# Kernel optimization log

Measured on AMD Instinct MI355X. Metric: run time of the kernel, lower is better.

The kernel has to match this reference:

```python
import jax, jax.numpy as jnp
import numpy as np

R = 8192        # rays
S_C = 64        # coarse samples per ray
S_F = 128       # fine samples per ray
NEAR, FAR = 2.0, 6.0
HIDDEN = 64
WHITE_BKGD = True
EPS_T = 1e-10   # transmittance eps (matches volumetric_rendering)
EPS_W = 1e-5    # weight-sum padding eps (matches piecewise_constant_pdf)


def setup_inputs() -> dict:
    key = jax.random.key(0)
    k0, k1, k2, k3, k4, k5 = jax.random.split(key, 6)
    return {
        "ray_origins": jax.random.normal(k0, (R, 3), jnp.float32),
        "ray_directions": jax.random.normal(k1, (R, 3), jnp.float32),
        "W1": jax.random.normal(k2, (6, HIDDEN), jnp.float32) * 0.5,
        "b1": jax.random.normal(k3, (HIDDEN,), jnp.float32) * 0.1,
        "W2": jax.random.normal(k4, (HIDDEN, 4), jnp.float32) * 0.3,
        "b2": jax.random.normal(k5, (4,), jnp.float32) * 0.1,
    }


def _mlp(coords, viewdirs, W1, b1, W2, b2):
    # coords: [R,S,3], viewdirs: [R,3] -> raw_rgb [R,S,3], raw_sigma [R,S]
    vd = jnp.broadcast_to(viewdirs[:, None, :], coords.shape)
    x = jnp.concatenate([coords, vd], axis=-1)            # [R,S,6]
    h = jax.nn.relu(jnp.einsum('rsi,ih->rsh', x, W1) + b1)
    out = jnp.einsum('rsh,ho->rso', h, W2) + b2           # [R,S,4]
    return out[..., :3], out[..., 3]


def _volrender(rgb, sigma, z_vals, directions):
    # rgb [R,S,3], sigma [R,S], z_vals [R,S], directions [R,3]
    dists = (z_vals[:, 1:] - z_vals[:, :-1]) * jnp.linalg.norm(directions, axis=-1, keepdims=True)
    alpha = 1.0 - jnp.exp(-sigma[:, :-1] * dists)         # [R,S-1]
    trans = jnp.concatenate([jnp.ones_like(alpha[:, :1]),
                             jnp.cumprod(1.0 - alpha + EPS_T, axis=-1)], axis=-1)
    alpha = jnp.concatenate([alpha, jnp.ones_like(alpha[:, :1])], axis=-1)
    weights = alpha * trans                               # [R,S]
    comp_rgb = jnp.einsum('rs,rsc->rc', weights, rgb)
    acc = weights.sum(-1)
    depth = (weights * z_vals).sum(-1)
    if WHITE_BKGD:
        comp_rgb = comp_rgb + (1.0 - acc)[:, None]
    return comp_rgb, weights, depth


def _piecewise_constant_pdf(bins, weights, num_samples):
    # bins [R,B+1], weights [R,B]; deterministic branch (randomized=False)
    nbins = weights.shape[-1]
    wsum = weights.sum(-1, keepdims=True)
    padding = jnp.maximum(0.0, EPS_W - wsum)
    weights = weights + padding / nbins
    wsum = wsum + padding
    pdf = weights / wsum
    cdf = jnp.minimum(1.0, jnp.cumsum(pdf[:, :-1], axis=-1))
    cdf = jnp.concatenate([jnp.zeros_like(cdf[:, :1]), cdf, jnp.ones_like(cdf[:, :1])], axis=-1)  # [R,B+1]
    u = jnp.linspace(0.0, 1.0 - jnp.finfo(jnp.float32).eps, num_samples)  # [F]
    mask = u[None, None, :] >= cdf[:, :, None]            # [R,B+1,F]

    def find_interval(x):  # x [R,B+1]
        x0 = jnp.max(jnp.where(mask, x[:, :, None], x[:, :1, None]), axis=1)
        x1 = jnp.min(jnp.where(~mask, x[:, :, None], x[:, -1:, None]), axis=1)
        return x0, x1

    bins_g0, bins_g1 = find_interval(bins)
    cdf_g0, cdf_g1 = find_interval(cdf)
    t = jnp.clip(jnp.nan_to_num((u[None, :] - cdf_g0) / (cdf_g1 - cdf_g0), nan=0.0), 0.0, 1.0)
    return jax.lax.stop_gradient(bins_g0 + t * (bins_g1 - bins_g0))  # [R,F]


def reference(ray_origins, ray_directions, W1, b1, W2, b2):
    Rn = ray_origins.shape[0]
    viewdirs = ray_directions / jnp.linalg.norm(ray_directions, axis=-1, keepdims=True)
    # coarse stratification (lindisp=False, randomized=False)
    t = jnp.linspace(0.0, 1.0, S_C)
    z_vals = jnp.broadcast_to(NEAR * (1.0 - t) + FAR * t, (Rn, S_C))
    coords = ray_origins[:, None, :] + z_vals[..., None] * ray_directions[:, None, :]
    raw_rgb, raw_sigma = _mlp(coords, viewdirs, W1, b1, W2, b2)
    rgb, sigma = jax.nn.sigmoid(raw_rgb), jax.nn.relu(raw_sigma)
    coarse_rgb, weights, coarse_depth = _volrender(rgb, sigma, z_vals, ray_directions)
    # hierarchical fine sampling via inverse-CDF over midpoint bins
    z_mid = 0.5 * (z_vals[:, 1:] + z_vals[:, :-1])
    z_samples = _piecewise_constant_pdf(z_mid, weights[:, 1:-1], S_F)
    z_fine = jnp.sort(jnp.concatenate([z_vals, z_samples], axis=-1), axis=-1)  # [R,S_C+S_F]
    coords = ray_origins[:, None, :] + z_fine[..., None] * ray_directions[:, None, :]
    # source falls through to coarse_model in the non-stateful branch; we mirror that (same MLP)
    raw_rgb, raw_sigma = _mlp(coords, viewdirs, W1, b1, W2, b2)
    rgb, sigma = jax.nn.sigmoid(raw_rgb), jax.nn.relu(raw_sigma)
    fine_rgb, _, fine_depth = _volrender(rgb, sigma, z_fine, ray_directions)
    return jnp.concatenate([coarse_rgb, coarse_depth[:, None], fine_rgb, fine_depth[:, None]], axis=-1)  # [R,8]
```

## Files before the change

### kernel.cpp

```cpp
#include <hip/hip_runtime.h>
#include <math.h>


#define RAYS   8192
#define NEARP  2.0f
#define FARP   6.0f
#define EPS_T  1e-10f
#define EPS_W  1e-5f
#define F32EPS 1.1920929e-7f

typedef float v2f __attribute__((ext_vector_type(2)));
__device__ __forceinline__ v2f mk2(float a, float b) { v2f r; r.x = a; r.y = b; return r; }
__device__ __forceinline__ v2f pfma(v2f a, v2f b, v2f c) { return __builtin_elementwise_fma(a, b, c); }
__device__ __forceinline__ v2f pmax0(v2f a) { return __builtin_elementwise_max(a, mk2(0.f, 0.f)); }

__device__ __forceinline__ float zc(int i) {
    const float t = (float)i * (1.0f / 63.0f);
    return NEARP * (1.0f - t) + FARP * t;
}
__device__ __forceinline__ float sigm(float x) { return 1.f / (1.f + __expf(-x)); }

__global__ __launch_bounds__(256) void nerf_kernel(
    const float* __restrict__ ro, const float* __restrict__ rd,
    const float* __restrict__ W1, const float* __restrict__ b1,
    const float* __restrict__ W2, const float* __restrict__ b2,
    float* __restrict__ out)
{
    __shared__ __align__(16) float sA[4][64];
    __shared__ __align__(16) float sB[4][64];
    __shared__ float sCdf[4][64];
    __shared__ float sZc [4][64];
    __shared__ float sZs [4][128];
    __shared__ float sZf [4][192];

    const int tid  = threadIdx.x;
    const int w    = tid >> 6;
    const int lane = tid & 63;
    const int ray  = blockIdx.x * 4 + w;

    const float ox = ro[ray * 3 + 0], oy = ro[ray * 3 + 1], oz = ro[ray * 3 + 2];
    const float dx = rd[ray * 3 + 0], dy = rd[ray * 3 + 1], dz = rd[ray * 3 + 2];
    const float norm = sqrtf(dx * dx + dy * dy + dz * dz);
    const float inv  = 1.f / norm;
    const float vx = dx * inv, vy = dy * inv, vz = dz * inv;

    {
        const float w10 = W1[lane],       w11 = W1[64 + lane],  w12 = W1[128 + lane];
        const float w13 = W1[192 + lane], w14 = W1[256 + lane], w15 = W1[320 + lane];
        float A = b1[lane];
        A = fmaf(vz, w15, A); A = fmaf(vy, w14, A); A = fmaf(vx, w13, A);
        A = fmaf(oz, w12, A); A = fmaf(oy, w11, A); A = fmaf(ox, w10, A);
        const float B = fmaf(dx, w10, fmaf(dy, w11, dz * w12));
        sA[w][lane] = A; sB[w][lane] = B;
    }
    __syncthreads();

    const float4* W2v = (const float4*)W2;
    const float bb0 = b2[0], bb1 = b2[1], bb2 = b2[2], bb3 = b2[3];

    const float z = zc(lane);
    sZc[w][lane] = z;
    const v2f zz = mk2(z, z);
    v2f o01 = mk2(bb0, bb1), o23 = mk2(bb2, bb3);
#pragma unroll 4
    for (int i = 0; i < 16; ++i) {
        const float4 a4 = ((const float4*)sA[w])[i];
        const float4 b4 = ((const float4*)sB[w])[i];
        const float4 q0 = W2v[4 * i + 0], q1 = W2v[4 * i + 1];
        const float4 q2 = W2v[4 * i + 2], q3 = W2v[4 * i + 3];
        const v2f hL = pmax0(pfma(zz, mk2(b4.x, b4.y), mk2(a4.x, a4.y)));
        const v2f hH = pmax0(pfma(zz, mk2(b4.z, b4.w), mk2(a4.z, a4.w)));
        o01 = pfma(mk2(hL.x, hL.x), mk2(q0.x, q0.y), o01);
        o23 = pfma(mk2(hL.x, hL.x), mk2(q0.z, q0.w), o23);
        o01 = pfma(mk2(hL.y, hL.y), mk2(q1.x, q1.y), o01);
        o23 = pfma(mk2(hL.y, hL.y), mk2(q1.z, q1.w), o23);
        o01 = pfma(mk2(hH.x, hH.x), mk2(q2.x, q2.y), o01);
        o23 = pfma(mk2(hH.x, hH.x), mk2(q2.z, q2.w), o23);
        o01 = pfma(mk2(hH.y, hH.y), mk2(q3.x, q3.y), o01);
        o23 = pfma(mk2(hH.y, hH.y), mk2(q3.z, q3.w), o23);
    }
    const float r   = sigm(o01.x), g = sigm(o01.y), bl = sigm(o23.x);
    const float sig = fmaxf(o23.y, 0.f);

    const float znext = __shfl_down(z, 1);
    const float dist  = (znext - z) * norm;
    const float alpha = (lane < 63) ? (1.f - __expf(-sig * dist)) : 1.f;
    const float vfac  = 1.f - alpha + EPS_T;
    float p = vfac;
#pragma unroll
    for (int off = 1; off < 64; off <<= 1) {
        const float q = __shfl_up(p, off);
        if (lane >= off) p *= q;
    }
    float excl = __shfl_up(p, 1);
    if (lane == 0) excl = 1.f;
    const float wgt = alpha * excl;

    float sr = wgt * r, sg = wgt * g, sb = wgt * bl, sd = wgt * z;
#pragma unroll
    for (int m = 1; m < 64; m <<= 1) {
        sr += __shfl_xor(sr, m); sg += __shfl_xor(sg, m);
        sb += __shfl_xor(sb, m); sd += __shfl_xor(sd, m);
    }

    const float wmraw = __shfl_down(wgt, 1);
    const float wmv   = (lane < 62) ? wmraw : 0.f;
    float wsum = wmv;
#pragma unroll
    for (int m = 1; m < 64; m <<= 1) wsum += __shfl_xor(wsum, m);
    const float pad  = fmaxf(0.f, EPS_W - wsum);
    const float wadj = wmv + pad * (1.0f / 62.0f);
    const float wsp  = wsum + pad;
    const float pdf  = (lane < 62) ? (wadj / wsp) : 0.f;
    float ps = pdf;
#pragma unroll
    for (int off = 1; off < 64; off <<= 1) {
        const float q = __shfl_up(ps, off);
        if (lane >= off) ps += q;
    }
    if (lane < 61)  sCdf[w][lane + 1] = fminf(1.f, ps);
    if (lane == 61) sCdf[w][0]  = 0.f;
    if (lane == 62) sCdf[w][62] = 1.f;
    __syncthreads();

    float zsv[2];
#pragma unroll
    for (int j = 0; j < 2; ++j) {
        const int f = lane * 2 + j;
        const float u = (float)f * ((1.0f - F32EPS) / 127.0f);
        int lo = 0, hi = 62;
        while (hi - lo > 1) {
            const int mid = (lo + hi) >> 1;
            if (sCdf[w][mid] <= u) lo = mid; else hi = mid;
        }
        const float c0 = sCdf[w][lo], c1 = sCdf[w][lo + 1];
        const float den = c1 - c0;
        float tt = (den > 0.f) ? (u - c0) / den : 0.f;
        tt = fminf(fmaxf(tt, 0.f), 1.f);
        const float za = zc(lo), zb = zc(lo + 1), zd = zc(lo + 2);
        const float bin0 = 0.5f * (za + zb), bin1 = 0.5f * (zb + zd);
        const float zs = fmaf(tt, bin1 - bin0, bin0);
        zsv[j] = zs;
        sZs[w][f] = zs;
    }
    __syncthreads();

    {
        int lo = 0, hi = 128;
        while (lo < hi) { const int mid = (lo + hi) >> 1; if (sZs[w][mid] < z) lo = mid + 1; else hi = mid; }
        sZf[w][lane + lo] = z;
    }
#pragma unroll
    for (int j = 0; j < 2; ++j) {
        const float bv = zsv[j];
        const int f = lane * 2 + j;
        int lo = 0, hi = 64;
        while (lo < hi) { const int mid = (lo + hi) >> 1; if (sZc[w][mid] <= bv) lo = mid + 1; else hi = mid; }
        sZf[w][f + lo] = bv;
    }
    __syncthreads();

    const float zf0 = sZf[w][3 * lane + 0];
    const float zf1 = sZf[w][3 * lane + 1];
    const float zf2 = sZf[w][3 * lane + 2];
    const float zn2 = sZf[w][min(3 * lane + 3, 191)];

    const v2f zA = mk2(zf0, zf0), zB = mk2(zf1, zf1), zC = mk2(zf2, zf2);
    v2f a01 = mk2(bb0, bb1), a23 = mk2(bb2, bb3);
    v2f e01 = mk2(bb0, bb1), e23 = mk2(bb2, bb3);
    v2f f01 = mk2(bb0, bb1), f23 = mk2(bb2, bb3);
#pragma unroll 2
    for (int i = 0; i < 16; ++i) {
        const float4 a4 = ((const float4*)sA[w])[i];
        const float4 b4 = ((const float4*)sB[w])[i];
        const float4 q0 = W2v[4 * i + 0], q1 = W2v[4 * i + 1];
        const float4 q2 = W2v[4 * i + 2], q3 = W2v[4 * i + 3];
        const v2f blo = mk2(b4.x, b4.y), bhi = mk2(b4.z, b4.w);
        const v2f alo = mk2(a4.x, a4.y), ahi = mk2(a4.z, a4.w);
        const v2f hAL = pmax0(pfma(zA, blo, alo)), hAH = pmax0(pfma(zA, bhi, ahi));
        const v2f hBL = pmax0(pfma(zB, blo, alo)), hBH = pmax0(pfma(zB, bhi, ahi));
        const v2f hCL = pmax0(pfma(zC, blo, alo)), hCH = pmax0(pfma(zC, bhi, ahi));
        const v2f q0a = mk2(q0.x, q0.y), q0b = mk2(q0.z, q0.w);
        const v2f q1a = mk2(q1.x, q1.y), q1b = mk2(q1.z, q1.w);
        const v2f q2a = mk2(q2.x, q2.y), q2b = mk2(q2.z, q2.w);
        const v2f q3a = mk2(q3.x, q3.y), q3b = mk2(q3.z, q3.w);
        a01 = pfma(mk2(hAL.x, hAL.x), q0a, a01); a23 = pfma(mk2(hAL.x, hAL.x), q0b, a23);
        a01 = pfma(mk2(hAL.y, hAL.y), q1a, a01); a23 = pfma(mk2(hAL.y, hAL.y), q1b, a23);
        a01 = pfma(mk2(hAH.x, hAH.x), q2a, a01); a23 = pfma(mk2(hAH.x, hAH.x), q2b, a23);
        a01 = pfma(mk2(hAH.y, hAH.y), q3a, a01); a23 = pfma(mk2(hAH.y, hAH.y), q3b, a23);
        e01 = pfma(mk2(hBL.x, hBL.x), q0a, e01); e23 = pfma(mk2(hBL.x, hBL.x), q0b, e23);
        e01 = pfma(mk2(hBL.y, hBL.y), q1a, e01); e23 = pfma(mk2(hBL.y, hBL.y), q1b, e23);
        e01 = pfma(mk2(hBH.x, hBH.x), q2a, e01); e23 = pfma(mk2(hBH.x, hBH.x), q2b, e23);
        e01 = pfma(mk2(hBH.y, hBH.y), q3a, e01); e23 = pfma(mk2(hBH.y, hBH.y), q3b, e23);
        f01 = pfma(mk2(hCL.x, hCL.x), q0a, f01); f23 = pfma(mk2(hCL.x, hCL.x), q0b, f23);
        f01 = pfma(mk2(hCL.y, hCL.y), q1a, f01); f23 = pfma(mk2(hCL.y, hCL.y), q1b, f23);
        f01 = pfma(mk2(hCH.x, hCH.x), q2a, f01); f23 = pfma(mk2(hCH.x, hCH.x), q2b, f23);
        f01 = pfma(mk2(hCH.y, hCH.y), q3a, f01); f23 = pfma(mk2(hCH.y, hCH.y), q3b, f23);
    }
    const float r0s = sigm(a01.x), g0s = sigm(a01.y), b0s = sigm(a23.x), s0 = fmaxf(a23.y, 0.f);
    const float r1s = sigm(e01.x), g1s = sigm(e01.y), b1s = sigm(e23.x), s1 = fmaxf(e23.y, 0.f);
    const float r2s = sigm(f01.x), g2s = sigm(f01.y), b2s = sigm(f23.x), s2 = fmaxf(f23.y, 0.f);

    const float d0 = (zf1 - zf0) * norm, d1 = (zf2 - zf1) * norm, d2 = (zn2 - zf2) * norm;
    const float al0 = 1.f - __expf(-s0 * d0);
    const float al1 = 1.f - __expf(-s1 * d1);
    const float al2 = (lane < 63) ? (1.f - __expf(-s2 * d2)) : 1.f;
    const float v0 = 1.f - al0 + EPS_T, v1 = 1.f - al1 + EPS_T, v2 = 1.f - al2 + EPS_T;

    float lp = v0 * v1 * v2;
#pragma unroll
    for (int off = 1; off < 64; off <<= 1) {
        const float q = __shfl_up(lp, off);
        if (lane >= off) lp *= q;
    }
    float ex = __shfl_up(lp, 1);
    if (lane == 0) ex = 1.f;
    const float tr1 = ex * v0, tr2 = tr1 * v1;
    const float w0 = al0 * ex, w1 = al1 * tr1, w2 = al2 * tr2;

    float fr = fmaf(w0, r0s, fmaf(w1, r1s, w2 * r2s));
    float fg = fmaf(w0, g0s, fmaf(w1, g1s, w2 * g2s));
    float fb = fmaf(w0, b0s, fmaf(w1, b1s, w2 * b2s));
    float fd = fmaf(w0, zf0, fmaf(w1, zf1, w2 * zf2));
#pragma unroll
    for (int m = 1; m < 64; m <<= 1) {
        fr += __shfl_xor(fr, m); fg += __shfl_xor(fg, m);
        fb += __shfl_xor(fb, m); fd += __shfl_xor(fd, m);
    }

    if (lane == 0) {
        float* po = out + (size_t)ray * 8;
        po[0] = sr; po[1] = sg; po[2] = sb; po[3] = sd;
        po[4] = fr; po[5] = fg; po[6] = fb; po[7] = fd;
    }
}

extern "C" void kernel_launch(void* const* d_in, const int* in_sizes, int n_in,
                              void* d_out, int out_size, void* d_ws, size_t ws_size,
                              hipStream_t stream) {
    const float* ro = (const float*)d_in[0];
    const float* rd = (const float*)d_in[1];
    const float* W1 = (const float*)d_in[2];
    const float* b1 = (const float*)d_in[3];
    const float* W2 = (const float*)d_in[4];
    const float* b2 = (const float*)d_in[5];
    float* out = (float*)d_out;
    nerf_kernel<<<dim3(RAYS / 4), dim3(256), 0, stream>>>(ro, rd, W1, b1, W2, b2, out);
}
```

Baseline: 90.30 us.

## Reuse coarse MLP outputs for fine pass and replace block barriers with wave syncs

The fine pass now evaluates the MLP only at the 128 new samples, two per lane. The 64 coarse-sample results (r, g, bl, sig from the coarse pass) are scattered with their z values into a per-wave shared pool in sorted order, so the 192-point volume render reads colour and density back from shared memory instead of recomputing all points. This removes about a third of the fine-pass MLP work. Block-wide __syncthreads are replaced by per-wave LDS waits plus wave barriers, since each wave owns one ray's shared data. The cost is extra shared-memory traffic, a larger LDS footprint from the 3 KB-per-wave pool, and reliance on wave-local synchronisation being sufficient.

```diff
diff --git a/kernel.cpp b/kernel.cpp
--- a/kernel.cpp
+++ b/kernel.cpp
@@ -19,6 +19,11 @@
     return NEARP * (1.0f - t) + FARP * t;
 }
 __device__ __forceinline__ float sigm(float x) { return 1.f / (1.f + __expf(-x)); }
+
+__device__ __forceinline__ void wsync() {
+    __asm__ __volatile__("s_waitcnt lgkmcnt(0)" ::: "memory");
+    __builtin_amdgcn_wave_barrier();
+}
 
 __global__ __launch_bounds__(256) void nerf_kernel(
     const float* __restrict__ ro, const float* __restrict__ rd,
@@ -28,15 +33,18 @@
 {
     __shared__ __align__(16) float sA[4][64];
     __shared__ __align__(16) float sB[4][64];
-    __shared__ float sCdf[4][64];
     __shared__ float sZc [4][64];
     __shared__ float sZs [4][128];
     __shared__ float sZf [4][192];
+    __shared__ __align__(16) char sPool[4][192 * 16];
 
     const int tid  = threadIdx.x;
     const int w    = tid >> 6;
     const int lane = tid & 63;
     const int ray  = blockIdx.x * 4 + w;
+
+    float*  sCdfw = (float*)&sPool[w][0];
+    float4* sValw = (float4*)&sPool[w][0];
 
     const float ox = ro[ray * 3 + 0], oy = ro[ray * 3 + 1], oz = ro[ray * 3 + 2];
     const float dx = rd[ray * 3 + 0], dy = rd[ray * 3 + 1], dz = rd[ray * 3 + 2];
@@ -53,7 +61,7 @@
         const float B = fmaf(dx, w10, fmaf(dy, w11, dz * w12));
         sA[w][lane] = A; sB[w][lane] = B;
     }
-    __syncthreads();
+    wsync();
 
     const float4* W2v = (const float4*)W2;
     const float bb0 = b2[0], bb1 = b2[1], bb2 = b2[2], bb3 = b2[3];
@@ -118,10 +126,10 @@
         const float q = __shfl_up(ps, off);
         if (lane >= off) ps += q;
     }
-    if (lane < 61)  sCdf[w][lane + 1] = fminf(1.f, ps);
-    if (lane == 61) sCdf[w][0]  = 0.f;
-    if (lane == 62) sCdf[w][62] = 1.f;
-    __syncthreads();
+    if (lane < 61)  sCdfw[lane + 1] = fminf(1.f, ps);
+    if (lane == 61) sCdfw[0]  = 0.f;
+    if (lane == 62) sCdfw[62] = 1.f;
+    wsync();
 
     float zsv[2];
 #pragma unroll
@@ -131,9 +139,9 @@
         int lo = 0, hi = 62;
         while (hi - lo > 1) {
             const int mid = (lo + hi) >> 1;
-            if (sCdf[w][mid] <= u) lo = mid; else hi = mid;
+            if (sCdfw[mid] <= u) lo = mid; else hi = mid;
         }
-        const float c0 = sCdf[w][lo], c1 = sCdf[w][lo + 1];
+        const float c0 = sCdfw[lo], c1 = sCdfw[lo + 1];
         const float den = c1 - c0;
         float tt = (den > 0.f) ? (u - c0) / den : 0.f;
         tt = fminf(fmaxf(tt, 0.f), 1.f);
@@ -143,32 +151,11 @@
         zsv[j] = zs;
         sZs[w][f] = zs;
     }
-    __syncthreads();
-
-    {
-        int lo = 0, hi = 128;
-        while (lo < hi) { const int mid = (lo + hi) >> 1; if (sZs[w][mid] < z) lo = mid + 1; else hi = mid; }
-        sZf[w][lane + lo] = z;
-    }
-#pragma unroll
-    for (int j = 0; j < 2; ++j) {
-        const float bv = zsv[j];
-        const int f = lane * 2 + j;
-        int lo = 0, hi = 64;
-        while (lo < hi) { const int mid = (lo + hi) >> 1; if (sZc[w][mid] <= bv) lo = mid + 1; else hi = mid; }
-        sZf[w][f + lo] = bv;
-    }
-    __syncthreads();
-
-    const float zf0 = sZf[w][3 * lane + 0];
-    const float zf1 = sZf[w][3 * lane + 1];
-    const float zf2 = sZf[w][3 * lane + 2];
-    const float zn2 = sZf[w][min(3 * lane + 3, 191)];
-
-    const v2f zA = mk2(zf0, zf0), zB = mk2(zf1, zf1), zC = mk2(zf2, zf2);
+    wsync();
+
+    const v2f zA = mk2(zsv[0], zsv[0]), zB = mk2(zsv[1], zsv[1]);
     v2f a01 = mk2(bb0, bb1), a23 = mk2(bb2, bb3);
     v2f e01 = mk2(bb0, bb1), e23 = mk2(bb2, bb3);
-    v2f f01 = mk2(bb0, bb1), f23 = mk2(bb2, bb3);
 #pragma unroll 2
     for (int i = 0; i < 16; ++i) {
         const float4 a4 = ((const float4*)sA[w])[i];
@@ -179,7 +166,6 @@
         const v2f alo = mk2(a4.x, a4.y), ahi = mk2(a4.z, a4.w);
         const v2f hAL = pmax0(pfma(zA, blo, alo)), hAH = pmax0(pfma(zA, bhi, ahi));
         const v2f hBL = pmax0(pfma(zB, blo, alo)), hBH = pmax0(pfma(zB, bhi, ahi));
-        const v2f hCL = pmax0(pfma(zC, blo, alo)), hCH = pmax0(pfma(zC, bhi, ahi));
         const v2f q0a = mk2(q0.x, q0.y), q0b = mk2(q0.z, q0.w);
         const v2f q1a = mk2(q1.x, q1.y), q1b = mk2(q1.z, q1.w);
         const v2f q2a = mk2(q2.x, q2.y), q2b = mk2(q2.z, q2.w);
@@ -192,22 +178,46 @@
         e01 = pfma(mk2(hBL.y, hBL.y), q1a, e01); e23 = pfma(mk2(hBL.y, hBL.y), q1b, e23);
         e01 = pfma(mk2(hBH.x, hBH.x), q2a, e01); e23 = pfma(mk2(hBH.x, hBH.x), q2b, e23);
         e01 = pfma(mk2(hBH.y, hBH.y), q3a, e01); e23 = pfma(mk2(hBH.y, hBH.y), q3b, e23);
-        f01 = pfma(mk2(hCL.x, hCL.x), q0a, f01); f23 = pfma(mk2(hCL.x, hCL.x), q0b, f23);
-        f01 = pfma(mk2(hCL.y, hCL.y), q1a, f01); f23 = pfma(mk2(hCL.y, hCL.y), q1b, f23);
-        f01 = pfma(mk2(hCH.x, hCH.x), q2a, f01); f23 = pfma(mk2(hCH.x, hCH.x), q2b, f23);
-        f01 = pfma(mk2(hCH.y, hCH.y), q3a, f01); f23 = pfma(mk2(hCH.y, hCH.y), q3b, f23);
     }
     const float r0s = sigm(a01.x), g0s = sigm(a01.y), b0s = sigm(a23.x), s0 = fmaxf(a23.y, 0.f);
     const float r1s = sigm(e01.x), g1s = sigm(e01.y), b1s = sigm(e23.x), s1 = fmaxf(e23.y, 0.f);
-    const float r2s = sigm(f01.x), g2s = sigm(f01.y), b2s = sigm(f23.x), s2 = fmaxf(f23.y, 0.f);
+
+    {
+        int lo = 0, hi = 128;
+        while (lo < hi) { const int mid = (lo + hi) >> 1; if (sZs[w][mid] < z) lo = mid + 1; else hi = mid; }
+        sZf[w][lane + lo] = z;
+        float4 cv; cv.x = r; cv.y = g; cv.z = bl; cv.w = sig;
+        sValw[lane + lo] = cv;
+    }
+#pragma unroll
+    for (int j = 0; j < 2; ++j) {
+        const float bv = zsv[j];
+        const int f = lane * 2 + j;
+        int lo = 0, hi = 64;
+        while (lo < hi) { const int mid = (lo + hi) >> 1; if (sZc[w][mid] <= bv) lo = mid + 1; else hi = mid; }
+        sZf[w][f + lo] = bv;
+        float4 cv;
+        if (j == 0) { cv.x = r0s; cv.y = g0s; cv.z = b0s; cv.w = s0; }
+        else        { cv.x = r1s; cv.y = g1s; cv.z = b1s; cv.w = s1; }
+        sValw[f + lo] = cv;
+    }
+    wsync();
+
+    const float zf0 = sZf[w][3 * lane + 0];
+    const float zf1 = sZf[w][3 * lane + 1];
+    const float zf2 = sZf[w][3 * lane + 2];
+    const float zn2 = sZf[w][min(3 * lane + 3, 191)];
+    const float4 c4a = sValw[3 * lane + 0];
+    const float4 c4b = sValw[3 * lane + 1];
+    const float4 c4c = sValw[3 * lane + 2];
 
     const float d0 = (zf1 - zf0) * norm, d1 = (zf2 - zf1) * norm, d2 = (zn2 - zf2) * norm;
-    const float al0 = 1.f - __expf(-s0 * d0);
-    const float al1 = 1.f - __expf(-s1 * d1);
-    const float al2 = (lane < 63) ? (1.f - __expf(-s2 * d2)) : 1.f;
-    const float v0 = 1.f - al0 + EPS_T, v1 = 1.f - al1 + EPS_T, v2 = 1.f - al2 + EPS_T;
-
-    float lp = v0 * v1 * v2;
+    const float al0 = 1.f - __expf(-c4a.w * d0);
+    const float al1 = 1.f - __expf(-c4b.w * d1);
+    const float al2 = (lane < 63) ? (1.f - __expf(-c4c.w * d2)) : 1.f;
+    const float t0v = 1.f - al0 + EPS_T, t1v = 1.f - al1 + EPS_T, t2v = 1.f - al2 + EPS_T;
+
+    float lp = t0v * t1v * t2v;
 #pragma unroll
     for (int off = 1; off < 64; off <<= 1) {
         const float q = __shfl_up(lp, off);
@@ -215,13 +225,13 @@
     }
     float ex = __shfl_up(lp, 1);
     if (lane == 0) ex = 1.f;
-    const float tr1 = ex * v0, tr2 = tr1 * v1;
+    const float tr1 = ex * t0v, tr2 = tr1 * t1v;
     const float w0 = al0 * ex, w1 = al1 * tr1, w2 = al2 * tr2;
 
-    float fr = fmaf(w0, r0s, fmaf(w1, r1s, w2 * r2s));
-    float fg = fmaf(w0, g0s, fmaf(w1, g1s, w2 * g2s));
-    float fb = fmaf(w0, b0s, fmaf(w1, b1s, w2 * b2s));
-    float fd = fmaf(w0, zf0, fmaf(w1, zf1, w2 * zf2));
+    float fr = fmaf(w0, c4a.x, fmaf(w1, c4b.x, w2 * c4c.x));
+    float fg = fmaf(w0, c4a.y, fmaf(w1, c4b.y, w2 * c4c.y));
+    float fb = fmaf(w0, c4a.z, fmaf(w1, c4b.z, w2 * c4c.z));
+    float fd = fmaf(w0, zf0,   fmaf(w1, zf1,   w2 * zf2));
 #pragma unroll
     for (int m = 1; m < 64; m <<= 1) {
         fr += __shfl_xor(fr, m); fg += __shfl_xor(fg, m);
```

Measured after the change: 85.69 us. -5.1%, faster.
